# Optimization experiments

Hardware: AMD Instinct MI355X
Metric: run time of the kernel (lower is better)

## Reference

```python
import jax, jax.numpy as jnp
import numpy as np

LATENT_SHAPES = [(192, 2, 2), (48, 4, 4), (24, 8, 8), (12, 16, 16), (6, 32, 32)]
B = 4          # batch
M = 32         # num_bases
HT, WT = 32, 32  # target spatial size = spatial size of z[-1] = (H/2, W/2)
EPS = 1e-3
CT = sum(s[0] for s in LATENT_SHAPES)  # 282


def _forward_fft(zs):
    # strided zero-insertion upsample of each latent to (HT, WT), concat channels, 2D FFT
    ups = []
    for zi in zs:
        b, c, h, w = zi.shape
        rh, rw = HT // h, WT // w
        u = jnp.zeros((b, c, HT, WT), zi.dtype).at[..., ::rh, ::rw].set(zi)
        ups.append(u)
    z = jnp.concatenate(ups, axis=1)            # (B, CT, HT, WT)
    return jnp.fft.fftn(z, axes=(-2, -1))       # complex64


def _inverse_fft(v_fft):
    # inverse FFT, take real part, split channels per level, strided downsample
    v = jnp.fft.ifftn(v_fft, axes=(-2, -1)).real  # (B, M, CT, HT, WT)
    splits = np.cumsum([s[0] for s in LATENT_SHAPES])[:-1]
    parts = jnp.split(v, splits, axis=-3)
    out = []
    for vi, (c, h, w) in zip(parts, LATENT_SHAPES):
        rh, rw = HT // h, WT // w
        out.append(vi[..., ::rh, ::rw])           # (B, M, c, h, w)
    return out


def _vector_field(zs, L, lam):
    z_fft = _forward_fft(zs)
    La = (L - jnp.swapaxes(L, -1, -2)).astype(jnp.complex64)        # antisymmetric (M, CT, CT)
    lam_a = (lam - jnp.roll(jnp.flip(lam, (1, 2)), (1, 1), axis=(1, 2))) * 1j  # (M, HT, WT) imaginary
    v_fft = jnp.einsum('mcd,bchw->bmdhw', La, z_fft)                 # (B, M, CT, HT, WT) complex
    v_fft = v_fft * lam_a[None, :, None, :, :]
    return _inverse_fft(v_fft)


def _log_prob(ws, zs, L, lam):
    S_ww = sum(jnp.einsum('bchw,bchw->b', wi, wi) for wi in ws)      # (B,)
    v = _vector_field(zs, L, lam)
    S_zz = sum(jnp.einsum('bnchw,bmchw->bnm', vi, vi) for vi in v)   # (B, M, M)
    S_zw = sum(jnp.einsum('bnchw,bchw->bn', vi, wi) for vi, wi in zip(v, ws))  # (B, M)
    var = jnp.maximum(jnp.mean(jnp.diagonal(S_zz, axis1=-2, axis2=-1), -1), 1e-6)
    std = jnp.sqrt(var)
    S_zz = S_zz / var[:, None, None]
    S_zw = S_zw / std[:, None]
    I = jnp.eye(M, dtype=S_zz.dtype)
    Mm = S_zz + EPS * I
    trace = EPS * S_ww + jnp.einsum('bn,bn->b', S_zw, S_zw)
    Lh = jnp.linalg.cholesky(Mm)
    logdet = 2.0 * jnp.sum(jnp.log(jnp.diagonal(Lh, axis1=-2, axis2=-1)), -1)
    return 0.5 * (logdet - trace)


def setup_inputs() -> dict:
    key = jax.random.key(0)
    ks = jax.random.split(key, 12)
    inp = {}
    for i, (c, h, w) in enumerate(LATENT_SHAPES):
        inp[f'z{i}'] = jax.random.normal(ks[i], (B, c, h, w), jnp.float32)
        inp[f'w{i}'] = jax.random.normal(ks[5 + i], (B, c, h, w), jnp.float32)
    inp['L'] = jax.random.normal(ks[10], (M, CT, CT), jnp.float32) * np.float32(1.0 / np.sqrt(CT))
    inp['lam'] = jax.random.normal(ks[11], (M, HT, WT), jnp.float32)
    return inp


def reference(z0, z1, z2, z3, z4, w0, w1, w2, w3, w4, L, lam):
    return _log_prob([w0, w1, w2, w3, w4], [z0, z1, z2, z3, z4], L, lam)
```

## Files before the change

### kernel.cpp

```cpp
#include <hip/hip_runtime.h>
#include <math.h>

#define NB 4
#define NM 32
#define CTOT 282
#define EPSV 1e-3f

__constant__ int g_cL[5]   = {192,48,24,12,6};
__constant__ int g_hL[5]   = {2,4,8,16,32};
__constant__ int g_coff[5] = {0,192,240,264,276};
__constant__ int g_zo[5]   = {0,768,1536,3072,6144};
__constant__ int g_po[4]   = {0,4,20,84};

__constant__ int t_lo[48] = {0,0,0,0,0,0,0,0,0,0,0,0,0,0,0,0,
                             0,0,0,0,0,0,0,0,0,0,0,0,0,0,0,0,
                             1,1,1,1,1,1,1,1, 2,2,2,2, 3,3, 4,4};
__constant__ int t_d0[48] = {0,6,12,18,24,30,36,42,48,54,60,66,72,78,84,90,
                             96,102,108,114,120,126,132,138,144,150,156,162,168,174,180,186,
                             192,198,204,210,216,222,228,234, 240,246,252,258, 264,270, 276,279};
__constant__ int t_nd[48] = {6,6,6,6,6,6,6,6,6,6,6,6,6,6,6,6,
                             6,6,6,6,6,6,6,6,6,6,6,6,6,6,6,6,
                             6,6,6,6,6,6,6,6, 6,6,6,6, 6,6, 3,3};

__constant__ int dft_l[30]  = {0,0,0, 1,1,1, 2,2,2,2,2,2,
                               3,3,3,3,3,3,3,3,3,3,3,3, 4,4,4,4,4,4};
__constant__ int dft_c0[30] = {0,64,128, 0,16,32, 0,4,8,12,16,20,
                               0,1,2,3,4,5,6,7,8,9,10,11, 0,1,2,3,4,5};
__constant__ int dft_nc[30] = {64,64,64, 16,16,16, 4,4,4,4,4,4,
                               1,1,1,1,1,1,1,1,1,1,1,1, 1,1,1,1,1,1};

#define N_LA     (NM*CTOT*CTOT)
#define OFF_LAT  0
#define OFF_ZRE  (OFF_LAT + N_LA)
#define OFF_ZIM  (OFF_ZRE + NB*12288)
#define OFF_WRE  (OFF_ZIM + NB*12288)
#define OFF_WIM  (OFF_WRE + NB*12288)
#define OFF_LAM  (OFF_WIM + NB*12288)
#define OFF_LAMF (OFF_LAM + NM*1024)
#define OFF_UR   (OFF_LAMF + NM*340)
#define OFF_UI   (OFF_UR + NB*NM*6*340)
#define OFF_VRE  (OFF_UI + NB*NM*6*340)
#define OFF_VIM  (OFF_VRE + NB*NM*12288)
#define OFF_SZZ  (OFF_VIM + NB*NM*12288)
#define OFF_SZW  (OFF_SZZ + NB*NM*NM)
#define OFF_SWW  (OFF_SZW + NB*NM)

#define PRE_LAT   (NM*81)
#define PRE_LAMF  (PRE_LAT + NM)
#define PRE_DFT   (PRE_LAMF + 2*NB*30)
#define PRE_SWW   (PRE_DFT + NB)
#define PRE_ZERO  (PRE_SWW + 17)

__global__ void __launch_bounds__(256) k_pre(
    const float* z0,const float* z1,const float* z2,const float* z3,const float* z4,
    const float* w0,const float* w1,const float* w2,const float* w3,const float* w4,
    const float* __restrict__ L, const float* __restrict__ lam, float* __restrict__ ws){
  __shared__ float shm[3136];
  int bid = blockIdx.x, t = threadIdx.x;
  if (bid < PRE_LAT){
    float* A  = shm;
    float* Bt = shm + 1056;
    int m = bid/81; int tl = bid%81;
    int d0 = (tl/9)*32, c0 = (tl%9)*32;
    const float* Lm = L + (size_t)m*CTOT*CTOT;
    for (int i=t;i<1024;i+=256){
      int r=i>>5, c=i&31;
      A[r*33+c]  = (c0+r<CTOT && d0+c<CTOT) ? Lm[(c0+r)*CTOT + d0+c] : 0.f;
      Bt[r*33+c] = (d0+r<CTOT && c0+c<CTOT) ? Lm[(d0+r)*CTOT + c0+c] : 0.f;
    }
    __syncthreads();
    float* out = ws + OFF_LAT + (size_t)m*CTOT*CTOT;
    for (int i=t;i<1024;i+=256){
      int r=i>>5, c=i&31;
      if (d0+r<CTOT && c0+c<CTOT)
        out[(size_t)(d0+r)*CTOT + c0+c] = A[c*33+r] - Bt[r*33+c];
    }
    return;
  }
  if (bid < PRE_LAMF){
    float* sA = shm;
    float* f3 = shm + 1024;
    float* f2 = shm + 1280;
    float* f1 = shm + 1344;
    int m = bid - PRE_LAT;
    for (int k=t;k<1024;k+=256){
      int ky=k>>5, kx=k&31;
      int nk = (((32-ky)&31)<<5) | ((32-kx)&31);
      float v = lam[(m<<10)+k] - lam[(m<<10)+nk];
      sA[k]=v;
      ws[OFF_LAM+(m<<10)+k]=v;
    }
    __syncthreads();
    { int s=t; int ky=s>>4, kx=s&15;
      float v = sA[(ky<<5)+kx]+sA[((ky+16)<<5)+kx]+sA[(ky<<5)+kx+16]+sA[((ky+16)<<5)+kx+16];
      f3[s]=v; ws[OFF_LAMF+m*340+84+s]=v; }
    __syncthreads();
    if (t<64){ int ky=t>>3, kx=t&7;
      float v = f3[(ky<<4)+kx]+f3[((ky+8)<<4)+kx]+f3[(ky<<4)+kx+8]+f3[((ky+8)<<4)+kx+8];
      f2[t]=v; ws[OFF_LAMF+m*340+20+t]=v; }
    __syncthreads();
    if (t<16){ int ky=t>>2, kx=t&3;
      float v = f2[(ky<<3)+kx]+f2[((ky+4)<<3)+kx]+f2[(ky<<3)+kx+4]+f2[((ky+4)<<3)+kx+4];
      f1[t]=v; ws[OFF_LAMF+m*340+4+t]=v; }
    __syncthreads();
    if (t<4){ int ky=t>>1, kx=t&1;
      float v = f1[(ky<<2)+kx]+f1[((ky+2)<<2)+kx]+f1[(ky<<2)+kx+2]+f1[((ky+2)<<2)+kx+2];
      ws[OFF_LAMF+m*340+t]=v; }
    return;
  }
  if (bid < PRE_DFT){
    float* sIn = shm;
    float* s1r = shm + 1024;
    float* s1i = shm + 2048;
    float* lc  = shm + 3072;
    float* lsn = shm + 3104;
    int i0 = bid - PRE_LAMF;
    int which = i0 / (NB*30);
    int rem = i0 % (NB*30);
    int b = rem / 30, j = rem % 30;
    int l = dft_l[j], c0 = dft_c0[j], nc = dft_nc[j];
    int h = g_hL[l], n = h*h;
    int elems = nc*n;
    const float* src;
    switch (which*5 + l){
      case 0: src=z0; break; case 1: src=z1; break; case 2: src=z2; break;
      case 3: src=z3; break; case 4: src=z4; break;
      case 5: src=w0; break; case 6: src=w1; break; case 7: src=w2; break;
      case 8: src=w3; break; default: src=w4; break;
    }
    for (int i=t;i<elems;i+=256) sIn[i] = src[(b*g_cL[l] + c0)*n + i];
    if (t<h){
      float ang = -6.2831853071795864f * (float)t / (float)h;
      lc[t] = cosf(ang); lsn[t] = sinf(ang);
    }
    __syncthreads();
    for (int p=t;p<elems;p+=256){
      int p2=p%n, cc=p/n;
      int y=p2/h, kx=p2-y*h;
      float re=0.f, im=0.f;
      for (int x=0;x<h;x++){
        int id = (kx*x)%h;
        float v = sIn[cc*n + y*h + x];
        re += v*lc[id]; im += v*lsn[id];
      }
      s1r[p]=re; s1i[p]=im;
    }
    __syncthreads();
    float scale = which ? 1.0f/(float)h : 1.0f;
    float* outR = ws + (which?OFF_WRE:OFF_ZRE) + b*12288 + g_zo[l] + c0*n;
    float* outI = ws + (which?OFF_WIM:OFF_ZIM) + b*12288 + g_zo[l] + c0*n;
    for (int p=t;p<elems;p+=256){
      int p2=p%n, cc=p/n;
      int ky=p2/h, kx=p2-(p2/h)*h;
      float re=0.f, im=0.f;
      for (int y=0;y<h;y++){
        int id=(ky*y)%h;
        float c=lc[id], s=lsn[id];
        float ar=s1r[cc*n + y*h + kx], ai=s1i[cc*n + y*h + kx];
        re += ar*c - ai*s;
        im += ar*s + ai*c;
      }
      outR[p]=re*scale; outI[p]=im*scale;
    }
    return;
  }
  if (bid < PRE_SWW){
    float* red = shm;
    int b = bid - PRE_DFT;
    const float* ptr[5] = {w0,w1,w2,w3,w4};
    float s = 0.f;
    for (int l=0;l<5;l++){
      int sz = g_cL[l]*g_hL[l]*g_hL[l];
      const float* p = ptr[l] + b*sz;
      for (int i=t;i<sz;i+=256){ float v=p[i]; s += v*v; }
    }
    red[t]=s; __syncthreads();
    for (int o=128;o>0;o>>=1){ if (t<o) red[t]+=red[t+o]; __syncthreads(); }
    if (t==0) ws[OFF_SWW + b] = red[0];
    return;
  }
  int i = (bid - PRE_SWW)*256 + t;
  if (i < NB*NM*NM + NB*NM) ws[OFF_SZZ + i] = 0.f;
}

__global__ void k_u(float* __restrict__ ws){
  __shared__ float pr[1024], pi[1024], q3r[256],q3i[256],q2r[64],q2i[64],q1r[16],q1i[16];
  int bid = blockIdx.x, t = threadIdx.x;
  int c = bid%6; int m = (bid/6)%NM; int b = bid/(6*NM);
  const float* la = ws+OFF_LAM+(m<<10);
  const float* zr = ws+OFF_ZRE+b*12288+6144+(c<<10);
  const float* zi = ws+OFF_ZIM+b*12288+6144+(c<<10);
  for (int k=t;k<1024;k+=256){ float f=la[k]; pr[k]=f*zr[k]; pi[k]=f*zi[k]; }
  __syncthreads();
  size_t base = (size_t)((b*NM+m)*6+c)*340;
  float* UR = ws+OFF_UR+base; float* UI = ws+OFF_UI+base;
  { int s=t; int ky=s>>4, kx=s&15;
    float r = pr[(ky<<5)+kx]+pr[((ky+16)<<5)+kx]+pr[(ky<<5)+kx+16]+pr[((ky+16)<<5)+kx+16];
    float ii= pi[(ky<<5)+kx]+pi[((ky+16)<<5)+kx]+pi[(ky<<5)+kx+16]+pi[((ky+16)<<5)+kx+16];
    q3r[s]=r; q3i[s]=ii; UR[84+s]=r; UI[84+s]=ii; }
  __syncthreads();
  if (t<64){ int ky=t>>3, kx=t&7;
    float r = q3r[(ky<<4)+kx]+q3r[((ky+8)<<4)+kx]+q3r[(ky<<4)+kx+8]+q3r[((ky+8)<<4)+kx+8];
    float ii= q3i[(ky<<4)+kx]+q3i[((ky+8)<<4)+kx]+q3i[(ky<<4)+kx+8]+q3i[((ky+8)<<4)+kx+8];
    q2r[t]=r; q2i[t]=ii; UR[20+t]=r; UI[20+t]=ii; }
  __syncthreads();
  if (t<16){ int ky=t>>2, kx=t&3;
    float r = q2r[(ky<<3)+kx]+q2r[((ky+4)<<3)+kx]+q2r[(ky<<3)+kx+4]+q2r[((ky+4)<<3)+kx+4];
    float ii= q2i[(ky<<3)+kx]+q2i[((ky+4)<<3)+kx]+q2i[(ky<<3)+kx+4]+q2i[((ky+4)<<3)+kx+4];
    q1r[t]=r; q1i[t]=ii; UR[4+t]=r; UI[4+t]=ii; }
  __syncthreads();
  if (t<4){ int ky=t>>1, kx=t&1;
    float r = q1r[(ky<<2)+kx]+q1r[((ky+2)<<2)+kx]+q1r[(ky<<2)+kx+2]+q1r[((ky+2)<<2)+kx+2];
    float ii= q1i[(ky<<2)+kx]+q1i[((ky+2)<<2)+kx]+q1i[(ky<<2)+kx+2]+q1i[((ky+2)<<2)+kx+2];
    UR[t]=r; UI[t]=ii; }
}

__global__ void __launch_bounds__(256) k_fold(float* __restrict__ ws){
  __shared__ float smem[6160];
  float* pre   = smem;
  float* pim   = smem + 2040;
  float* sLa   = smem + 4080;
  float* c64r  = smem + 4080;
  float* c64i  = smem + 4464;
  float* c16r  = smem + 4848;
  float* c16i  = smem + 4944;
  float* c4r   = smem + 5040;
  float* c4i   = smem + 5064;
  float* lamf  = smem + 5784;
  float* ssla  = smem + 6124;

  int t = threadIdx.x, bid = blockIdx.x;
  int m    = bid / (NB*48);
  int rem  = bid % (NB*48);
  int b    = rem / 48;
  int tile = rem % 48;
  int lo = t_lo[tile], d0 = t_d0[tile], nd = t_nd[tile];
  int ho = g_hL[lo];
  int nbins = ho*ho;
  const float* zreb = ws + OFF_ZRE + b*12288;
  const float* zimb = ws + OFF_ZIM + b*12288;
  const float* latm = ws + OFF_LAT + (size_t)m*CTOT*CTOT;

  for (int i=t;i<340;i+=256) lamf[i] = ws[OFF_LAMF + m*340 + i];
  for (int i=t;i<nd*282;i+=256){ int d=i/282, c=i-d*282; sLa[d*284+c] = latm[(size_t)(d0+d)*CTOT + c]; }
  if (t<nd*6){ int d=t/6, c=t-d*6; ssla[t] = latm[(size_t)(d0+d)*CTOT + 276 + c]; }

  int lA, kkA, c0A, nA, offP; bool wrt;
  if (t<64){ lA=0; kkA=t&3; c0A=(t>>2)*12; nA=4; offP=0; wrt=(t<4); }
  else if (t<128){ int i=t-64; lA=1; kkA=i&15; c0A=(i>>4)*12; nA=16; offP=4; wrt=(i<16); }
  else { int i=t-128; lA=2; kkA=i>>1; c0A=(i&1)*12; nA=64; offP=20; wrt=((i&1)==0); }
  float zAr[12], zAi[12], zBr[12], zBi[12];
  {
    const float* zr = zreb + g_zo[lA] + kkA;
    const float* zi = zimb + g_zo[lA] + kkA;
    #pragma unroll
    for (int c=0;c<12;c++){ zAr[c]=zr[(c0A+c)*nA]; zAi[c]=zi[(c0A+c)*nA]; }
    const float* zr3 = zreb + 3072 + t;
    const float* zi3 = zimb + 3072 + t;
    #pragma unroll
    for (int c=0;c<12;c++){ zBr[c]=zr3[c*256]; zBi[c]=zi3[c*256]; }
  }
  __syncthreads();

  int offA = g_coff[lA] + c0A;
  for (int d=0; d<nd; d++){
    const float4* laA = (const float4*)(sLa + d*284 + offA);
    const float4* laB = (const float4*)(sLa + d*284 + 264);
    float4 a0=laA[0], a1=laA[1], a2=laA[2];
    float4 b0=laB[0], b1=laB[1], b2=laB[2];
    float av[12] = {a0.x,a0.y,a0.z,a0.w, a1.x,a1.y,a1.z,a1.w, a2.x,a2.y,a2.z,a2.w};
    float bv[12] = {b0.x,b0.y,b0.z,b0.w, b1.x,b1.y,b1.z,b1.w, b2.x,b2.y,b2.z,b2.w};
    float prA=0.f, piA=0.f, prB=0.f, piB=0.f;
    #pragma unroll
    for (int c=0;c<12;c++){ prA+=av[c]*zAr[c]; piA+=av[c]*zAi[c]; }
    #pragma unroll
    for (int c=0;c<12;c++){ prB+=bv[c]*zBr[c]; piB+=bv[c]*zBi[c]; }
    if (t<64){
      prA += __shfl_xor(prA, 4);  piA += __shfl_xor(piA, 4);
      prA += __shfl_xor(prA, 8);  piA += __shfl_xor(piA, 8);
      prA += __shfl_xor(prA,16);  piA += __shfl_xor(piA,16);
      prA += __shfl_xor(prA,32);  piA += __shfl_xor(piA,32);
    } else if (t<128){
      prA += __shfl_xor(prA,16);  piA += __shfl_xor(piA,16);
      prA += __shfl_xor(prA,32);  piA += __shfl_xor(piA,32);
    } else {
      prA += __shfl_xor(prA, 1);  piA += __shfl_xor(piA, 1);
    }
    if (wrt){ pre[d*340+offP+kkA]=prA; pim[d*340+offP+kkA]=piA; }
    pre[d*340+84+t]=prB; pim[d*340+84+t]=piB;
  }
  __syncthreads();

  float sc = (float)ho/1024.f;
  if (lo==4){
    int dlb = d0 - 276;
    const float* lamA = ws + OFF_LAM + (m<<10);
    float* vRb = ws + OFF_VRE + (size_t)(b*NM+m)*12288 + 6144 + (dlb<<10);
    float* vIb = ws + OFF_VIM + (size_t)(b*NM+m)*12288 + 6144 + (dlb<<10);
    const float* z4r = zreb + 6144;
    const float* z4i = zimb + 6144;
    for (int q=t; q<1024; q+=256){
      int ky=q>>5, kx=q&31;
      int a0=((ky&1)<<1)|(kx&1);
      int a1=4+(((ky&3)<<2)|(kx&3));
      int a2=20+(((ky&7)<<3)|(kx&7));
      int a3=84+(((ky&15)<<4)|(kx&15));
      float zr_[6], zi_[6];
      #pragma unroll
      for (int c=0;c<6;c++){ zr_[c]=z4r[(c<<10)+q]; zi_[c]=z4i[(c<<10)+q]; }
      float lm = lamA[q]*sc;
      for (int d=0; d<nd; d++){
        const float* pd = pre + d*340; const float* qd = pim + d*340;
        float Br = pd[a0]+pd[a1]+pd[a2]+pd[a3];
        float Bi = qd[a0]+qd[a1]+qd[a2]+qd[a3];
        #pragma unroll
        for (int c=0;c<6;c++){ float a=ssla[d*6+c]; Br+=a*zr_[c]; Bi+=a*zi_[c]; }
        vRb[(d<<10)+q] = -lm*Bi;
        vIb[(d<<10)+q] =  lm*Br;
      }
    }
    return;
  }

  if (lo<3){
    for (int idx=t; idx<nd*64; idx+=256){
      int d=idx>>6, k2=idx&63, ky=k2>>3, kx=k2&7;
      const float* pd = pre + d*340 + 84; const float* qd = pim + d*340 + 84;
      float r=0.f, ii=0.f;
      #pragma unroll
      for (int jy=0;jy<2;jy++)
        #pragma unroll
        for (int jx=0;jx<2;jx++){
          int a = ((ky+8*jy)<<4) | (kx+8*jx);
          float f = lamf[84+a];
          r += f*pd[a]; ii += f*qd[a];
        }
      if (lo<2){ float f=lamf[20+k2]; r+=f*pre[d*340+20+k2]; ii+=f*pim[d*340+20+k2]; }
      c64r[idx]=r; c64i[idx]=ii;
    }
  }
  __syncthreads();
  if (lo<2){
    for (int idx=t; idx<nd*16; idx+=256){
      int d=idx>>4, k2=idx&15, ky=k2>>2, kx=k2&3, base=d<<6;
      float r = c64r[base+(ky<<3)+kx]+c64r[base+((ky+4)<<3)+kx]+c64r[base+(ky<<3)+kx+4]+c64r[base+((ky+4)<<3)+kx+4];
      float ii= c64i[base+(ky<<3)+kx]+c64i[base+((ky+4)<<3)+kx]+c64i[base+(ky<<3)+kx+4]+c64i[base+((ky+4)<<3)+kx+4];
      if (lo<1){ float f=lamf[4+k2]; r+=f*pre[d*340+4+k2]; ii+=f*pim[d*340+4+k2]; }
      c16r[idx]=r; c16i[idx]=ii;
    }
  }
  __syncthreads();
  if (lo==0 && t<nd*4){
    int d=t>>2, k2=t&3, ky=k2>>1, kx=k2&1, base=d<<4;
    c4r[t]=c16r[base+(ky<<2)+kx]+c16r[base+((ky+2)<<2)+kx]+c16r[base+(ky<<2)+kx+2]+c16r[base+((ky+2)<<2)+kx+2];
    c4i[t]=c16i[base+(ky<<2)+kx]+c16i[base+((ky+2)<<2)+kx]+c16i[base+(ky<<2)+kx+2]+c16i[base+((ky+2)<<2)+kx+2];
  }
  __syncthreads();

  int dlb = d0 - g_coff[lo];
  float* vRb = ws + OFF_VRE + (size_t)(b*NM+m)*12288 + g_zo[lo];
  float* vIb = ws + OFF_VIM + (size_t)(b*NM+m)*12288 + g_zo[lo];
  const float* URg = ws + OFF_UR + (size_t)((b*NM+m)*6)*340 + g_po[lo];
  const float* UIg = ws + OFF_UI + (size_t)((b*NM+m)*6)*340 + g_po[lo];
  for (int idx=t; idx<nd*nbins; idx+=256){
    int d=idx/nbins, bin=idx-d*nbins;
    int ky=bin/ho, kx=bin-ky*ho;
    const float* pd = pre + d*340; const float* qd = pim + d*340;
    float Br = pd[((ky&1)<<1)|(kx&1)], Bi = qd[((ky&1)<<1)|(kx&1)];
    if (lo>=1){ int ix=4+(((ky&3)<<2)|(kx&3)); Br+=pd[ix]; Bi+=qd[ix]; }
    if (lo>=2){ int ix=20+(((ky&7)<<3)|(kx&7)); Br+=pd[ix]; Bi+=qd[ix]; }
    if (lo>=3){ int ix=84+(((ky&15)<<4)|(kx&15)); Br+=pd[ix]; Bi+=qd[ix]; }
    float lf = lamf[g_po[lo]+bin];
    float Vr = lf*Br, Vi = lf*Bi;
    if (lo==2){ Vr+=c64r[(d<<6)+bin]; Vi+=c64i[(d<<6)+bin]; }
    else if (lo==1){ Vr+=c16r[(d<<4)+bin]; Vi+=c16i[(d<<4)+bin]; }
    else if (lo==0){ Vr+=c4r[(d<<2)+bin]; Vi+=c4i[(d<<2)+bin]; }
    #pragma unroll
    for (int c=0;c<6;c++){ float a=ssla[d*6+c]; Vr+=a*URg[c*340+bin]; Vi+=a*UIg[c*340+bin]; }
    int ob = (dlb+d)*nbins + bin;
    vRb[ob] = -sc*Vi;
    vIb[ob] =  sc*Vr;
  }
}

__global__ void __launch_bounds__(256) k_gram(float* __restrict__ ws){
  __shared__ float tile[32*132];
  __shared__ float wv[128];
  int t = threadIdx.x;
  int bid = blockIdx.x;
  int b = bid / 192, ch = bid % 192;
  int half = ch / 96;
  int k0 = (ch % 96) * 128;
  const float* V = ws + (half?OFF_VIM:OFF_VRE);
  const float* W = ws + (half?OFF_WIM:OFF_WRE) + b*12288 + k0;
  #pragma unroll
  for (int p=0;p<4;p++){
    int i4 = t + (p<<8);
    int row = i4 >> 5, c4 = i4 & 31;
    float4 v = *(const float4*)(V + (size_t)(b*NM+row)*12288 + k0 + (c4<<2));
    *(float4*)(tile + row*132 + (c4<<2)) = v;
  }
  if (t<128) wv[t] = W[t];
  __syncthreads();
  const float4* tf = (const float4*)tile;
  int n0 = t>>5, mm = t&31;
  float acc0=0.f, acc1=0.f, acc2=0.f, acc3=0.f;
  const float4* rm = tf + mm*33;
  const float4* r0 = tf + n0*33;
  const float4* r1 = tf + (n0+8)*33;
  const float4* r2 = tf + (n0+16)*33;
  const float4* r3 = tf + (n0+24)*33;
  for (int k4=0;k4<32;k4++){
    float4 vm = rm[k4];
    float4 v0 = r0[k4];
    float4 v1 = r1[k4];
    float4 v2 = r2[k4];
    float4 v3 = r3[k4];
    acc0 += v0.x*vm.x + v0.y*vm.y + v0.z*vm.z + v0.w*vm.w;
    acc1 += v1.x*vm.x + v1.y*vm.y + v1.z*vm.z + v1.w*vm.w;
    acc2 += v2.x*vm.x + v2.y*vm.y + v2.z*vm.z + v2.w*vm.w;
    acc3 += v3.x*vm.x + v3.y*vm.y + v3.z*vm.z + v3.w*vm.w;
  }
  float* szz = ws + OFF_SZZ + (b<<10);
  atomicAdd(&szz[(n0<<5) + mm], acc0);
  atomicAdd(&szz[((n0+8)<<5) + mm], acc1);
  atomicAdd(&szz[((n0+16)<<5) + mm], acc2);
  atomicAdd(&szz[((n0+24)<<5) + mm], acc3);
  if (t < 32){
    const float4* rn = tf + t*33;
    const float4* wf = (const float4*)wv;
    float acc=0.f;
    for (int k4=0;k4<32;k4++){
      float4 a = rn[k4]; float4 wq = wf[k4];
      acc += a.x*wq.x + a.y*wq.y + a.z*wq.z + a.w*wq.w;
    }
    atomicAdd(&ws[OFF_SZW + (b<<5) + t], acc);
  }
}

__global__ void k_final(float* __restrict__ ws, float* __restrict__ out){
  __shared__ float A[32][33];
  __shared__ float svar;
  int b = blockIdx.x, t = threadIdx.x;
  const float* szz = ws + OFF_SZZ + (b<<10);
  if (t==0){
    float s=0.f;
    for (int i=0;i<32;i++) s += szz[i*33];
    svar = fmaxf(s/32.0f, 1e-6f);
  }
  __syncthreads();
  float var = svar;
  for (int i=t;i<1024;i+=64){
    int r=i>>5, c=i&31;
    A[r][c] = szz[i]/var + ((r==c)?EPSV:0.0f);
  }
  __syncthreads();
  for (int j=0;j<32;j++){
    if (t==0) A[j][j] = sqrtf(A[j][j]);
    __syncthreads();
    if (t>j && t<32) A[t][j] /= A[j][j];
    __syncthreads();
    if (t>j && t<32){
      float lij = A[t][j];
      for (int k=j+1;k<=t;k++) A[t][k] -= lij*A[k][j];
    }
    __syncthreads();
  }
  if (t==0){
    float logdet=0.f;
    for (int j=0;j<32;j++) logdet += logf(A[j][j]);
    logdet *= 2.0f;
    const float* szw = ws + OFF_SZW + (b<<5);
    float s2=0.f;
    for (int n=0;n<32;n++) s2 += szw[n]*szw[n];
    float trace = EPSV*ws[OFF_SWW + b] + s2/var;
    out[b] = 0.5f*(logdet - trace);
  }
}

extern "C" void kernel_launch(void* const* d_in, const int* in_sizes, int n_in,
                              void* d_out, int out_size, void* d_ws, size_t ws_size,
                              hipStream_t stream){
  const float* z0 = (const float*)d_in[0];
  const float* w0 = (const float*)d_in[1];
  const float* z1 = (const float*)d_in[2];
  const float* w1 = (const float*)d_in[3];
  const float* z2 = (const float*)d_in[4];
  const float* w2 = (const float*)d_in[5];
  const float* z3 = (const float*)d_in[6];
  const float* w3 = (const float*)d_in[7];
  const float* z4 = (const float*)d_in[8];
  const float* w4 = (const float*)d_in[9];
  const float* L   = (const float*)d_in[10];
  const float* lam = (const float*)d_in[11];
  float* ws = (float*)d_ws;
  float* out = (float*)d_out;

  k_pre<<<PRE_ZERO, 256, 0, stream>>>(z0,z1,z2,z3,z4,w0,w1,w2,w3,w4, L, lam, ws);
  k_u<<<NB*NM*6, 256, 0, stream>>>(ws);
  k_fold<<<NB*NM*48, 256, 0, stream>>>(ws);
  k_gram<<<NB*192, 256, 0, stream>>>(ws);
  k_final<<<NB, 64, 0, stream>>>(ws, out);
}
```

Baseline: 206.0 us.

## Store z-FFT and U buffers channel-innermost for vectorized loads in fold kernel

The forward DFT now writes z spectra for levels 0-3 in bin-major, channel-innermost order. The U partial sums are stored as 8-wide channel-padded vectors per bin. This lets k_fold fetch its 12 channel values and 6 U values with float4 loads instead of strided scalar gathers. The cost is strided scattered writes in k_pre and k_u, plus a wider U buffer.

```diff
diff --git a/kernel.cpp b/kernel.cpp
--- a/kernel.cpp
+++ b/kernel.cpp
@@ -38,8 +38,8 @@
 #define OFF_LAM  (OFF_WIM + NB*12288)
 #define OFF_LAMF (OFF_LAM + NM*1024)
 #define OFF_UR   (OFF_LAMF + NM*340)
-#define OFF_UI   (OFF_UR + NB*NM*6*340)
-#define OFF_VRE  (OFF_UI + NB*NM*6*340)
+#define OFF_UI   (OFF_UR + NB*NM*2720)
+#define OFF_VRE  (OFF_UI + NB*NM*2720)
 #define OFF_VIM  (OFF_VRE + NB*NM*12288)
 #define OFF_SZZ  (OFF_VIM + NB*NM*12288)
 #define OFF_SZW  (OFF_SZZ + NB*NM*NM)
@@ -147,8 +147,9 @@
     }
     __syncthreads();
     float scale = which ? 1.0f/(float)h : 1.0f;
-    float* outR = ws + (which?OFF_WRE:OFF_ZRE) + b*12288 + g_zo[l] + c0*n;
-    float* outI = ws + (which?OFF_WIM:OFF_ZIM) + b*12288 + g_zo[l] + c0*n;
+    bool zt = (which==0 && l<4);
+    float* outR = ws + (which?OFF_WRE:OFF_ZRE) + b*12288 + g_zo[l];
+    float* outI = ws + (which?OFF_WIM:OFF_ZIM) + b*12288 + g_zo[l];
     for (int p=t;p<elems;p+=256){
       int p2=p%n, cc=p/n;
       int ky=p2/h, kx=p2-(p2/h)*h;
@@ -160,7 +161,8 @@
         re += ar*c - ai*s;
         im += ar*s + ai*c;
       }
-      outR[p]=re*scale; outI[p]=im*scale;
+      int o = zt ? (p2*g_cL[l] + c0 + cc) : ((c0+cc)*n + p2);
+      outR[o]=re*scale; outI[o]=im*scale;
     }
     return;
   }
@@ -192,27 +194,27 @@
   const float* zi = ws+OFF_ZIM+b*12288+6144+(c<<10);
   for (int k=t;k<1024;k+=256){ float f=la[k]; pr[k]=f*zr[k]; pi[k]=f*zi[k]; }
   __syncthreads();
-  size_t base = (size_t)((b*NM+m)*6+c)*340;
+  size_t base = (size_t)(b*NM+m)*2720;
   float* UR = ws+OFF_UR+base; float* UI = ws+OFF_UI+base;
   { int s=t; int ky=s>>4, kx=s&15;
     float r = pr[(ky<<5)+kx]+pr[((ky+16)<<5)+kx]+pr[(ky<<5)+kx+16]+pr[((ky+16)<<5)+kx+16];
     float ii= pi[(ky<<5)+kx]+pi[((ky+16)<<5)+kx]+pi[(ky<<5)+kx+16]+pi[((ky+16)<<5)+kx+16];
-    q3r[s]=r; q3i[s]=ii; UR[84+s]=r; UI[84+s]=ii; }
+    q3r[s]=r; q3i[s]=ii; UR[(84+s)*8+c]=r; UI[(84+s)*8+c]=ii; }
   __syncthreads();
   if (t<64){ int ky=t>>3, kx=t&7;
     float r = q3r[(ky<<4)+kx]+q3r[((ky+8)<<4)+kx]+q3r[(ky<<4)+kx+8]+q3r[((ky+8)<<4)+kx+8];
     float ii= q3i[(ky<<4)+kx]+q3i[((ky+8)<<4)+kx]+q3i[(ky<<4)+kx+8]+q3i[((ky+8)<<4)+kx+8];
-    q2r[t]=r; q2i[t]=ii; UR[20+t]=r; UI[20+t]=ii; }
+    q2r[t]=r; q2i[t]=ii; UR[(20+t)*8+c]=r; UI[(20+t)*8+c]=ii; }
   __syncthreads();
   if (t<16){ int ky=t>>2, kx=t&3;
     float r = q2r[(ky<<3)+kx]+q2r[((ky+4)<<3)+kx]+q2r[(ky<<3)+kx+4]+q2r[((ky+4)<<3)+kx+4];
     float ii= q2i[(ky<<3)+kx]+q2i[((ky+4)<<3)+kx]+q2i[(ky<<3)+kx+4]+q2i[((ky+4)<<3)+kx+4];
-    q1r[t]=r; q1i[t]=ii; UR[4+t]=r; UI[4+t]=ii; }
+    q1r[t]=r; q1i[t]=ii; UR[(4+t)*8+c]=r; UI[(4+t)*8+c]=ii; }
   __syncthreads();
   if (t<4){ int ky=t>>1, kx=t&1;
     float r = q1r[(ky<<2)+kx]+q1r[((ky+2)<<2)+kx]+q1r[(ky<<2)+kx+2]+q1r[((ky+2)<<2)+kx+2];
     float ii= q1i[(ky<<2)+kx]+q1i[((ky+2)<<2)+kx]+q1i[(ky<<2)+kx+2]+q1i[((ky+2)<<2)+kx+2];
-    UR[t]=r; UI[t]=ii; }
+    UR[t*8+c]=r; UI[t*8+c]=ii; }
 }
 
 __global__ void __launch_bounds__(256) k_fold(float* __restrict__ ws){
@@ -245,20 +247,26 @@
   for (int i=t;i<nd*282;i+=256){ int d=i/282, c=i-d*282; sLa[d*284+c] = latm[(size_t)(d0+d)*CTOT + c]; }
   if (t<nd*6){ int d=t/6, c=t-d*6; ssla[t] = latm[(size_t)(d0+d)*CTOT + 276 + c]; }
 
-  int lA, kkA, c0A, nA, offP; bool wrt;
-  if (t<64){ lA=0; kkA=t&3; c0A=(t>>2)*12; nA=4; offP=0; wrt=(t<4); }
-  else if (t<128){ int i=t-64; lA=1; kkA=i&15; c0A=(i>>4)*12; nA=16; offP=4; wrt=(i<16); }
-  else { int i=t-128; lA=2; kkA=i>>1; c0A=(i&1)*12; nA=64; offP=20; wrt=((i&1)==0); }
+  int lA, kkA, c0A, offP; bool wrt;
+  if (t<64){ lA=0; kkA=t&3; c0A=(t>>2)*12; offP=0; wrt=(t<4); }
+  else if (t<128){ int i=t-64; lA=1; kkA=i&15; c0A=(i>>4)*12; offP=4; wrt=(i<16); }
+  else { int i=t-128; lA=2; kkA=i>>1; c0A=(i&1)*12; offP=20; wrt=((i&1)==0); }
   float zAr[12], zAi[12], zBr[12], zBi[12];
   {
-    const float* zr = zreb + g_zo[lA] + kkA;
-    const float* zi = zimb + g_zo[lA] + kkA;
-    #pragma unroll
-    for (int c=0;c<12;c++){ zAr[c]=zr[(c0A+c)*nA]; zAi[c]=zi[(c0A+c)*nA]; }
-    const float* zr3 = zreb + 3072 + t;
-    const float* zi3 = zimb + 3072 + t;
-    #pragma unroll
-    for (int c=0;c<12;c++){ zBr[c]=zr3[c*256]; zBi[c]=zi3[c*256]; }
+    int oA = g_zo[lA] + kkA*g_cL[lA] + c0A;
+    const float4* zr4 = (const float4*)(zreb + oA);
+    const float4* zi4 = (const float4*)(zimb + oA);
+    float4 x0=zr4[0], x1=zr4[1], x2=zr4[2];
+    float4 y0=zi4[0], y1=zi4[1], y2=zi4[2];
+    zAr[0]=x0.x;zAr[1]=x0.y;zAr[2]=x0.z;zAr[3]=x0.w;zAr[4]=x1.x;zAr[5]=x1.y;zAr[6]=x1.z;zAr[7]=x1.w;zAr[8]=x2.x;zAr[9]=x2.y;zAr[10]=x2.z;zAr[11]=x2.w;
+    zAi[0]=y0.x;zAi[1]=y0.y;zAi[2]=y0.z;zAi[3]=y0.w;zAi[4]=y1.x;zAi[5]=y1.y;zAi[6]=y1.z;zAi[7]=y1.w;zAi[8]=y2.x;zAi[9]=y2.y;zAi[10]=y2.z;zAi[11]=y2.w;
+    int oB = 3072 + t*12;
+    const float4* zr3 = (const float4*)(zreb + oB);
+    const float4* zi3 = (const float4*)(zimb + oB);
+    float4 p0=zr3[0], p1=zr3[1], p2=zr3[2];
+    float4 q0=zi3[0], q1=zi3[1], q2=zi3[2];
+    zBr[0]=p0.x;zBr[1]=p0.y;zBr[2]=p0.z;zBr[3]=p0.w;zBr[4]=p1.x;zBr[5]=p1.y;zBr[6]=p1.z;zBr[7]=p1.w;zBr[8]=p2.x;zBr[9]=p2.y;zBr[10]=p2.z;zBr[11]=p2.w;
+    zBi[0]=q0.x;zBi[1]=q0.y;zBi[2]=q0.z;zBi[3]=q0.w;zBi[4]=q1.x;zBi[5]=q1.y;zBi[6]=q1.z;zBi[7]=q1.w;zBi[8]=q2.x;zBi[9]=q2.y;zBi[10]=q2.z;zBi[11]=q2.w;
   }
   __syncthreads();
 
@@ -360,8 +368,8 @@
   int dlb = d0 - g_coff[lo];
   float* vRb = ws + OFF_VRE + (size_t)(b*NM+m)*12288 + g_zo[lo];
   float* vIb = ws + OFF_VIM + (size_t)(b*NM+m)*12288 + g_zo[lo];
-  const float* URg = ws + OFF_UR + (size_t)((b*NM+m)*6)*340 + g_po[lo];
-  const float* UIg = ws + OFF_UI + (size_t)((b*NM+m)*6)*340 + g_po[lo];
+  const float* URg = ws + OFF_UR + (size_t)(b*NM+m)*2720;
+  const float* UIg = ws + OFF_UI + (size_t)(b*NM+m)*2720;
   for (int idx=t; idx<nd*nbins; idx+=256){
     int d=idx/nbins, bin=idx-d*nbins;
     int ky=bin/ho, kx=bin-ky*ho;
@@ -375,8 +383,16 @@
     if (lo==2){ Vr+=c64r[(d<<6)+bin]; Vi+=c64i[(d<<6)+bin]; }
     else if (lo==1){ Vr+=c16r[(d<<4)+bin]; Vi+=c16i[(d<<4)+bin]; }
     else if (lo==0){ Vr+=c4r[(d<<2)+bin]; Vi+=c4i[(d<<2)+bin]; }
-    #pragma unroll
-    for (int c=0;c<6;c++){ float a=ssla[d*6+c]; Vr+=a*URg[c*340+bin]; Vi+=a*UIg[c*340+bin]; }
+    {
+      int e = (g_po[lo]+bin)*8;
+      const float4* ur4 = (const float4*)(URg + e);
+      const float4* ui4 = (const float4*)(UIg + e);
+      float4 u0=ur4[0], u1=ur4[1];
+      float4 v0=ui4[0], v1=ui4[1];
+      const float* sd = ssla + d*6;
+      Vr += sd[0]*u0.x + sd[1]*u0.y + sd[2]*u0.z + sd[3]*u0.w + sd[4]*u1.x + sd[5]*u1.y;
+      Vi += sd[0]*v0.x + sd[1]*v0.y + sd[2]*v0.z + sd[3]*v0.w + sd[4]*v1.x + sd[5]*v1.y;
+    }
     int ob = (dlb+d)*nbins + bin;
     vRb[ob] = -sc*Vi;
     vIb[ob] =  sc*Vr;
```

New measurement: 208.5 us. No clear change (+1.2%).
